# Kernel tuning notes

Measured on AMD Instinct MI355X. Metric: run time of the kernel, lower is better.

Reference implementation:

```python
import jax, jax.numpy as jnp
import numpy as np

ALPHA = 0.2  # LeakyReLU negative slope
NEG_INF = -9e15


def gat_layer(h, adj_mask, W, a, concat):
    # h: [N, F_in], W: [F_in, F_out], a: [2*F_out, 1]
    Wh = h @ W                                   # [N, F_out]
    f_out = W.shape[1]
    e1 = Wh @ a[:f_out]                          # [N, 1]
    e2 = Wh @ a[f_out:]                          # [N, 1]
    e = jax.nn.leaky_relu(e1 + e2.T, ALPHA)      # [N, N] pairwise scores
    att = jnp.where(adj_mask, e, NEG_INF)
    att = jax.nn.softmax(att, axis=1)            # masked row softmax
    h_prime = att @ Wh                           # [N, F_out] aggregate
    out = jax.nn.elu(h_prime) if concat else h_prime
    return out, att


def setup_inputs() -> dict:
    N, nfeat, nhid, nclass = 8192, 512, 256, 16
    key = jax.random.key(0)
    k = jax.random.split(key, 6)
    x = jax.random.normal(k[0], (N, nfeat), dtype=jnp.float32)
    adj = jax.random.randint(k[1], (N, N), 0, 2, dtype=jnp.int32)
    W1 = jax.random.normal(k[2], (nfeat, nhid), dtype=jnp.float32) * (1.0 / np.sqrt(nfeat))
    a1 = jax.random.normal(k[3], (2 * nhid, 1), dtype=jnp.float32) * 0.1
    W2 = jax.random.normal(k[4], (nhid, nclass), dtype=jnp.float32) * (1.0 / np.sqrt(nhid))
    a2 = jax.random.normal(k[5], (2 * nclass, 1), dtype=jnp.float32) * 0.1
    return {"x": x, "adj": adj, "W1": W1, "a1": a1, "W2": W2, "a2": a2}


def reference(x, adj, W1, a1, W2, a2):
    adj_mask = adj > 0
    # layer 1: attentions (concat=True -> ELU)
    h1, att1 = gat_layer(x, adj_mask, W1, a1, concat=True)
    # out layer (concat=False) + sigmoid
    h2, att2 = gat_layer(h1, adj_mask, W2, a2, concat=False)
    out = jax.nn.sigmoid(h2)
    # mirrors torch return: (x, gft_list, att_list, attention)
    return out, h1, att1, att2
```

## Files before the change

### kernel.cpp

```cpp
#include <hip/hip_runtime.h>
#include <hip/hip_bf16.h>

#define LRELU_ALPHA 0.2f

typedef __attribute__((ext_vector_type(8))) __bf16 bf16x8;
typedef __attribute__((ext_vector_type(4))) float f32x4;
typedef __attribute__((ext_vector_type(8))) unsigned short u16x8;
typedef __attribute__((ext_vector_type(4))) unsigned short u16x4;

__device__ __forceinline__ unsigned short f2bf(float f) {
  unsigned int u = __float_as_uint(f);
  u += 0x7fffu + ((u >> 16) & 1u);
  return (unsigned short)(u >> 16);
}

__global__ __launch_bounds__(256) void gemm_f32_k(
    const float* __restrict__ A, const float* __restrict__ B,
    float* __restrict__ C, int M, int K, int Ncols)
{
  __shared__ float As[128][17];
  __shared__ float Bs[16][65];
  int t = threadIdx.x;
  int row0 = blockIdx.x * 128;
  int col0 = blockIdx.y * 64;
  int ty = t >> 4, tx = t & 15;
  float acc[8][4];
#pragma unroll
  for (int i = 0; i < 8; ++i)
#pragma unroll
    for (int j = 0; j < 4; ++j) acc[i][j] = 0.f;

  for (int kt = 0; kt < K; kt += 16) {
    __syncthreads();
    {
      int r = t >> 1, h = t & 1;
      const float4* src = (const float4*)(A + (size_t)(row0 + r) * K + kt + h * 8);
      float4 v0 = src[0], v1 = src[1];
      float* dst = &As[r][h * 8];
      dst[0]=v0.x; dst[1]=v0.y; dst[2]=v0.z; dst[3]=v0.w;
      dst[4]=v1.x; dst[5]=v1.y; dst[6]=v1.z; dst[7]=v1.w;
    }
    {
      int kr = t >> 4, seg = t & 15;
      const float4* src = (const float4*)(B + (size_t)(kt + kr) * Ncols + col0 + seg * 4);
      float4 v = src[0];
      float* dst = &Bs[kr][seg * 4];
      dst[0]=v.x; dst[1]=v.y; dst[2]=v.z; dst[3]=v.w;
    }
    __syncthreads();
#pragma unroll
    for (int k = 0; k < 16; ++k) {
      float bb[4];
#pragma unroll
      for (int j = 0; j < 4; ++j) bb[j] = Bs[k][tx * 4 + j];
#pragma unroll
      for (int i = 0; i < 8; ++i) {
        float aa = As[ty * 8 + i][k];
#pragma unroll
        for (int j = 0; j < 4; ++j) acc[i][j] = fmaf(aa, bb[j], acc[i][j]);
      }
    }
  }
#pragma unroll
  for (int i = 0; i < 8; ++i) {
    float4 v = make_float4(acc[i][0], acc[i][1], acc[i][2], acc[i][3]);
    *(float4*)(C + (size_t)(row0 + ty * 8 + i) * Ncols + col0 + tx * 4) = v;
  }
}

__global__ __launch_bounds__(256) void calc_e_k(
    const float* __restrict__ Wh, const float* __restrict__ a,
    float* __restrict__ e1, float* __restrict__ e2, int F)
{
  int row = blockIdx.x * 4 + (threadIdx.x >> 6);
  int l = threadIdx.x & 63;
  const float* r = Wh + (size_t)row * F;
  float s1 = 0.f, s2 = 0.f;
  for (int f = l; f < F; f += 64) {
    float v = r[f];
    s1 += v * a[f];
    s2 += v * a[F + f];
  }
#pragma unroll
  for (int off = 32; off; off >>= 1) {
    s1 += __shfl_down(s1, off);
    s2 += __shfl_down(s2, off);
  }
  if (l == 0) { e1[row] = s1; e2[row] = s2; }
}

__global__ void transpose_bf16_k(const float* __restrict__ in, unsigned short* __restrict__ out,
                                 int R, int Cc)
{
  __shared__ float tile[32][33];
  int tx = threadIdx.x, ty = threadIdx.y;
  int c0 = blockIdx.x * 32, r0 = blockIdx.y * 32;
  int c = c0 + tx;
  if (c < Cc) {
    for (int i = ty; i < 32; i += 8)
      tile[i][tx] = in[(size_t)(r0 + i) * Cc + c];
  }
  __syncthreads();
  int r = r0 + tx;
  for (int i = ty; i < 32; i += 8) {
    int cc = c0 + i;
    if (cc < Cc)
      out[(size_t)cc * R + r] = f2bf(tile[tx][i]);
  }
}

__global__ __launch_bounds__(256) void att_softmax1_k(
    const int* __restrict__ adj, const float* __restrict__ e1,
    const float* __restrict__ e2, float* __restrict__ att,
    unsigned* __restrict__ bits)
{
  __shared__ float red[4];
  int i = blockIdx.x, t = threadIdx.x;
  const int4* arow = (const int4*)(adj + (size_t)i * 8192);
  unsigned* brow = bits + (size_t)i * 256;
  float e1i = e1[i];
  float4 vv[8];
  float s = 0.f;
#pragma unroll
  for (int it = 0; it < 8; ++it) {
    int j4 = t + it * 256;
    int4 a4 = arow[j4];
    float4 ev = *(const float4*)(e2 + j4 * 4);
    unsigned n = (unsigned)(a4.x > 0) | ((unsigned)(a4.y > 0) << 1)
               | ((unsigned)(a4.z > 0) << 2) | ((unsigned)(a4.w > 0) << 3);
    unsigned v = n << ((t & 7) * 4);
    v |= __shfl_xor(v, 1);
    v |= __shfl_xor(v, 2);
    v |= __shfl_xor(v, 4);
    if ((t & 7) == 0) brow[it * 32 + (t >> 3)] = v;
    float e, p0, p1, p2, p3;
    e = e1i + ev.x; e = e > 0.f ? e : LRELU_ALPHA * e; p0 = (a4.x > 0) ? __expf(e) : 0.f;
    e = e1i + ev.y; e = e > 0.f ? e : LRELU_ALPHA * e; p1 = (a4.y > 0) ? __expf(e) : 0.f;
    e = e1i + ev.z; e = e > 0.f ? e : LRELU_ALPHA * e; p2 = (a4.z > 0) ? __expf(e) : 0.f;
    e = e1i + ev.w; e = e > 0.f ? e : LRELU_ALPHA * e; p3 = (a4.w > 0) ? __expf(e) : 0.f;
    vv[it] = make_float4(p0, p1, p2, p3);
    s += (p0 + p1) + (p2 + p3);
  }
#pragma unroll
  for (int off = 32; off; off >>= 1) s += __shfl_xor(s, off);
  if ((t & 63) == 0) red[t >> 6] = s;
  __syncthreads();
  s = red[0] + red[1] + red[2] + red[3];
  float inv = 1.f / s;
  float4* orow = (float4*)(att + (size_t)i * 8192);
#pragma unroll
  for (int it = 0; it < 8; ++it) {
    float4 p = vv[it];
    p.x *= inv; p.y *= inv; p.z *= inv; p.w *= inv;
    orow[t + it * 256] = p;
  }
}

__global__ __launch_bounds__(256) void att_softmax2_k(
    const unsigned* __restrict__ bits, const float* __restrict__ e1,
    const float* __restrict__ e2, float* __restrict__ att)
{
  __shared__ unsigned bw[256];
  __shared__ float red[4];
  int i = blockIdx.x, t = threadIdx.x;
  bw[t] = bits[(size_t)i * 256 + t];
  float e1i = e1[i];
  __syncthreads();
  float4 vv[8];
  float s = 0.f;
#pragma unroll
  for (int it = 0; it < 8; ++it) {
    int j4 = t + it * 256;
    float4 ev = *(const float4*)(e2 + j4 * 4);
    unsigned wb = bw[j4 >> 3];
    int b0 = (j4 & 7) * 4;
    float e, p0, p1, p2, p3;
    e = e1i + ev.x; e = e > 0.f ? e : LRELU_ALPHA * e; p0 = ((wb >> (b0 + 0)) & 1) ? __expf(e) : 0.f;
    e = e1i + ev.y; e = e > 0.f ? e : LRELU_ALPHA * e; p1 = ((wb >> (b0 + 1)) & 1) ? __expf(e) : 0.f;
    e = e1i + ev.z; e = e > 0.f ? e : LRELU_ALPHA * e; p2 = ((wb >> (b0 + 2)) & 1) ? __expf(e) : 0.f;
    e = e1i + ev.w; e = e > 0.f ? e : LRELU_ALPHA * e; p3 = ((wb >> (b0 + 3)) & 1) ? __expf(e) : 0.f;
    vv[it] = make_float4(p0, p1, p2, p3);
    s += (p0 + p1) + (p2 + p3);
  }
#pragma unroll
  for (int off = 32; off; off >>= 1) s += __shfl_xor(s, off);
  if ((t & 63) == 0) red[t >> 6] = s;
  __syncthreads();
  s = red[0] + red[1] + red[2] + red[3];
  float inv = 1.f / s;
  float4* orow = (float4*)(att + (size_t)i * 8192);
#pragma unroll
  for (int it = 0; it < 8; ++it) {
    float4 p = vv[it];
    p.x *= inv; p.y *= inv; p.z *= inv; p.w *= inv;
    orow[t + it * 256] = p;
  }
}

template<int BN, int SPLITK, int EPI>
__global__ __launch_bounds__(256) void gemm_mfma_k(
    const float* __restrict__ A, const unsigned short* __restrict__ BT,
    float* __restrict__ Cout, int M, int K, int ldc)
{
  constexpr int BM = 64, BK = 64;
  constexpr int WN = (BN == 64) ? 2 : 1;
  constexpr int WM = 4 / WN;
  constexpr int WROWS = BM / WM;
  constexpr int WCOLS = BN / WN;
  constexpr int FM = WROWS / 16;
  constexpr int FN = WCOLS / 16;
  __shared__ __align__(16) char As[BM * BK * 2];
  __shared__ __align__(16) char Bs[BN * BK * 2];
  int t = threadIdx.x;
  int row0 = blockIdx.x * BM;
  int col0 = blockIdx.y * BN;
  int ktiles = K / BK;
  int kt0 = blockIdx.z * (ktiles / SPLITK);
  int kt1 = kt0 + ktiles / SPLITK;
  int w = t >> 6, l = t & 63;
  int wm = w / WN, wn = w % WN;

  f32x4 acc[FM][FN] = {};

  int ar = t >> 2, aseg = t & 3;
  int swzA = (ar & 7) << 4;

  for (int kt = kt0; kt < kt1; ++kt) {
    __syncthreads();
    {
      const float4* src = (const float4*)(A + (size_t)(row0 + ar) * K + kt * BK + aseg * 16);
      float4 v0 = src[0], v1 = src[1], v2 = src[2], v3 = src[3];
      u16x8 c0, c1;
      c0[0]=f2bf(v0.x); c0[1]=f2bf(v0.y); c0[2]=f2bf(v0.z); c0[3]=f2bf(v0.w);
      c0[4]=f2bf(v1.x); c0[5]=f2bf(v1.y); c0[6]=f2bf(v1.z); c0[7]=f2bf(v1.w);
      c1[0]=f2bf(v2.x); c1[1]=f2bf(v2.y); c1[2]=f2bf(v2.z); c1[3]=f2bf(v2.w);
      c1[4]=f2bf(v3.x); c1[5]=f2bf(v3.y); c1[6]=f2bf(v3.z); c1[7]=f2bf(v3.w);
      int base = ar * 128 + aseg * 32;
      *(u16x8*)(As + ((base) ^ swzA)) = c0;
      *(u16x8*)(As + ((base + 16) ^ swzA)) = c1;
    }
    if (BN == 64) {
      int br = t >> 2, seg = t & 3;
      const u16x8* src = (const u16x8*)(BT + (size_t)(col0 + br) * K + kt * BK + seg * 16);
      u16x8 b0 = src[0], b1 = src[1];
      int base = br * 128 + seg * 32;
      int swz = (br & 7) << 4;
      *(u16x8*)(Bs + ((base) ^ swz)) = b0;
      *(u16x8*)(Bs + ((base + 16) ^ swz)) = b1;
    } else {
      int br = t >> 4, seg = t & 15;
      const u16x4* src = (const u16x4*)(BT + (size_t)(col0 + br) * K + kt * BK + seg * 4);
      u16x4 b0 = src[0];
      int base = br * 128 + seg * 8;
      int swz = (br & 7) << 4;
      *(u16x4*)(Bs + (base ^ swz)) = b0;
    }
    __syncthreads();
#pragma unroll
    for (int kk = 0; kk < BK; kk += 32) {
      bf16x8 af[FM], bfr[FN];
      int kb = (kk + (l >> 4) * 8) * 2;
#pragma unroll
      for (int fm = 0; fm < FM; ++fm) {
        int r = wm * WROWS + fm * 16 + (l & 15);
        af[fm] = *(const bf16x8*)(As + ((r * 128 + kb) ^ ((r & 7) << 4)));
      }
#pragma unroll
      for (int fn = 0; fn < FN; ++fn) {
        int c = wn * WCOLS + fn * 16 + (l & 15);
        bfr[fn] = *(const bf16x8*)(Bs + ((c * 128 + kb) ^ ((c & 7) << 4)));
      }
#pragma unroll
      for (int fm = 0; fm < FM; ++fm)
#pragma unroll
        for (int fn = 0; fn < FN; ++fn)
          acc[fm][fn] = __builtin_amdgcn_mfma_f32_16x16x32_bf16(af[fm], bfr[fn], acc[fm][fn], 0, 0, 0);
    }
  }
#pragma unroll
  for (int fm = 0; fm < FM; ++fm) {
#pragma unroll
    for (int fn = 0; fn < FN; ++fn) {
#pragma unroll
      for (int r = 0; r < 4; ++r) {
        int grow = row0 + wm * WROWS + fm * 16 + (l >> 4) * 4 + r;
        int gcol = col0 + wn * WCOLS + fn * 16 + (l & 15);
        float v = acc[fm][fn][r];
        if (EPI == 1) v = v > 0.f ? v : expm1f(v);
        size_t idx = (SPLITK > 1)
          ? ((size_t)blockIdx.z * M + grow) * ldc + gcol
          : (size_t)grow * ldc + gcol;
        Cout[idx] = v;
      }
    }
  }
}

__global__ __launch_bounds__(256) void gemm_small_k(
    const float* __restrict__ A, const float* __restrict__ B,
    float* __restrict__ C, int K, int Ncols)
{
  int t = threadIdx.x;
  int r = blockIdx.x * 16 + (t >> 4);
  int c = t & 15;
  const float* arow = A + (size_t)r * K;
  float acc = 0.f;
#pragma unroll 8
  for (int k = 0; k < K; ++k)
    acc = fmaf(arow[k], B[k * Ncols + c], acc);
  C[(size_t)r * Ncols + c] = acc;
}

__global__ void reduce_elu_k(const float* __restrict__ part, float* __restrict__ out, int total)
{
  int i = blockIdx.x * 256 + threadIdx.x;
  if (i < total) {
    float s = (part[i] + part[total + i]) + (part[2 * (size_t)total + i] + part[3 * (size_t)total + i]);
    out[i] = s > 0.f ? s : expm1f(s);
  }
}

__global__ void reduce_sig16_k(const float* __restrict__ part, float* __restrict__ out, int total)
{
  int i = blockIdx.x * 256 + threadIdx.x;
  if (i < total) {
    float s = 0.f;
#pragma unroll
    for (int z = 0; z < 16; ++z)
      s += part[(size_t)z * total + i];
    out[i] = 1.f / (1.f + __expf(-s));
  }
}

extern "C" void kernel_launch(void* const* d_in, const int* in_sizes, int n_in,
                              void* d_out, int out_size, void* d_ws, size_t ws_size,
                              hipStream_t stream)
{
  const float* x   = (const float*)d_in[0];
  const int*   adj = (const int*)d_in[1];
  const float* W1  = (const float*)d_in[2];
  const float* a1  = (const float*)d_in[3];
  const float* W2  = (const float*)d_in[4];
  const float* a2  = (const float*)d_in[5];

  float* out  = (float*)d_out;
  float* h1   = out + 131072;
  float* att1 = h1 + 2097152;
  float* att2 = att1 + 67108864;

  float* ws = (float*)d_ws;
  float* wh1 = ws;
  unsigned short* bt1 = (unsigned short*)(wh1 + 2097152);
  float* e1a = wh1 + 2097152 + 1048576;
  float* e2a = e1a + 8192;
  float* wh2 = e2a + 8192;
  unsigned short* bt2 = (unsigned short*)(wh2 + 131072);
  float* e1b = wh2 + 131072 + 65536;
  float* e2b = e1b + 8192;
  float* part2 = e2b + 8192;
  unsigned* bits = (unsigned*)(part2 + 2097152);
  float* part1 = (float*)(bits + 2097152);

  gemm_f32_k<<<dim3(64, 4), 256, 0, stream>>>(x, W1, wh1, 8192, 512, 256);
  calc_e_k<<<2048, 256, 0, stream>>>(wh1, a1, e1a, e2a, 256);
  transpose_bf16_k<<<dim3(8, 256), dim3(32, 8), 0, stream>>>(wh1, bt1, 8192, 256);
  att_softmax1_k<<<8192, 256, 0, stream>>>(adj, e1a, e2a, att1, bits);
  gemm_mfma_k<64, 4, 0><<<dim3(128, 4, 4), 256, 0, stream>>>(att1, bt1, part1, 8192, 8192, 256);
  reduce_elu_k<<<8192, 256, 0, stream>>>(part1, h1, 2097152);

  gemm_small_k<<<512, 256, 0, stream>>>(h1, W2, wh2, 256, 16);
  calc_e_k<<<2048, 256, 0, stream>>>(wh2, a2, e1b, e2b, 16);
  transpose_bf16_k<<<dim3(1, 256), dim3(32, 8), 0, stream>>>(wh2, bt2, 8192, 16);
  att_softmax2_k<<<8192, 256, 0, stream>>>(bits, e1b, e2b, att2);
  gemm_mfma_k<16, 16, 0><<<dim3(128, 1, 16), 256, 0, stream>>>(att2, bt2, part2, 8192, 8192, 16);
  reduce_sig16_k<<<512, 256, 0, stream>>>(part2, out, 131072);
}
```

Before: 460.8 us.

## Fuse layer-1 attention softmax into aggregation GEMM using a row-sum pre-pass

The layer-1 softmax kernel now only computes the packed adjacency bits and the inverse row sums. A new fused kernel rebuilds the normalized attention values from the bits, e1 and e2 tile by tile. It writes them to the att1 output and also converts them to bf16 in shared memory to feed MFMA directly, so the aggregation GEMM no longer reads the full fp32 att1 matrix back from memory. Split-K goes from 4 to 8, and the reduction kernel is adjusted to match. The exp work is done twice, the partial-sum buffer doubles, and the fused loop has no load/compute overlap.

```diff
diff --git a/kernel.cpp b/kernel.cpp
--- a/kernel.cpp
+++ b/kernel.cpp
@@ -109,17 +109,16 @@
   }
 }
 
-__global__ __launch_bounds__(256) void att_softmax1_k(
+__global__ __launch_bounds__(256) void rowsum_pack_k(
     const int* __restrict__ adj, const float* __restrict__ e1,
-    const float* __restrict__ e2, float* __restrict__ att,
-    unsigned* __restrict__ bits)
+    const float* __restrict__ e2, unsigned* __restrict__ bits,
+    float* __restrict__ sinv)
 {
   __shared__ float red[4];
   int i = blockIdx.x, t = threadIdx.x;
   const int4* arow = (const int4*)(adj + (size_t)i * 8192);
   unsigned* brow = bits + (size_t)i * 256;
   float e1i = e1[i];
-  float4 vv[8];
   float s = 0.f;
 #pragma unroll
   for (int it = 0; it < 8; ++it) {
@@ -133,26 +132,111 @@
     v |= __shfl_xor(v, 2);
     v |= __shfl_xor(v, 4);
     if ((t & 7) == 0) brow[it * 32 + (t >> 3)] = v;
-    float e, p0, p1, p2, p3;
-    e = e1i + ev.x; e = e > 0.f ? e : LRELU_ALPHA * e; p0 = (a4.x > 0) ? __expf(e) : 0.f;
-    e = e1i + ev.y; e = e > 0.f ? e : LRELU_ALPHA * e; p1 = (a4.y > 0) ? __expf(e) : 0.f;
-    e = e1i + ev.z; e = e > 0.f ? e : LRELU_ALPHA * e; p2 = (a4.z > 0) ? __expf(e) : 0.f;
-    e = e1i + ev.w; e = e > 0.f ? e : LRELU_ALPHA * e; p3 = (a4.w > 0) ? __expf(e) : 0.f;
-    vv[it] = make_float4(p0, p1, p2, p3);
-    s += (p0 + p1) + (p2 + p3);
+    float e;
+    e = e1i + ev.x; e = e > 0.f ? e : LRELU_ALPHA * e; s += (a4.x > 0) ? __expf(e) : 0.f;
+    e = e1i + ev.y; e = e > 0.f ? e : LRELU_ALPHA * e; s += (a4.y > 0) ? __expf(e) : 0.f;
+    e = e1i + ev.z; e = e > 0.f ? e : LRELU_ALPHA * e; s += (a4.z > 0) ? __expf(e) : 0.f;
+    e = e1i + ev.w; e = e > 0.f ? e : LRELU_ALPHA * e; s += (a4.w > 0) ? __expf(e) : 0.f;
   }
 #pragma unroll
   for (int off = 32; off; off >>= 1) s += __shfl_xor(s, off);
   if ((t & 63) == 0) red[t >> 6] = s;
   __syncthreads();
-  s = red[0] + red[1] + red[2] + red[3];
-  float inv = 1.f / s;
-  float4* orow = (float4*)(att + (size_t)i * 8192);
-#pragma unroll
-  for (int it = 0; it < 8; ++it) {
-    float4 p = vv[it];
-    p.x *= inv; p.y *= inv; p.z *= inv; p.w *= inv;
-    orow[t + it * 256] = p;
+  if (t == 0) sinv[i] = 1.f / (red[0] + red[1] + red[2] + red[3]);
+}
+
+__global__ __launch_bounds__(256) void fused_att_agg1_k(
+    const unsigned* __restrict__ bits, const float* __restrict__ e1,
+    const float* __restrict__ e2, const float* __restrict__ sinv,
+    const unsigned short* __restrict__ BT,
+    float* __restrict__ att, float* __restrict__ part)
+{
+  __shared__ __align__(16) char As[64 * 128];
+  __shared__ __align__(16) char Bs[256 * 128];
+  int t = threadIdx.x;
+  int l = t & 63, w = t >> 6;
+  int row0 = blockIdx.x * 64;
+  int z = blockIdx.y;
+  int wm = w >> 1, wn = w & 1;
+
+  f32x4 acc[2][8] = {};
+
+  int pr = t >> 2, seg = t & 3;
+  float e1v = e1[row0 + pr];
+  float siv = sinv[row0 + pr];
+  const unsigned* brow = bits + (size_t)(row0 + pr) * 256 + z * 32;
+  const float* e2p = e2 + z * 1024;
+  float* arow_att = att + (size_t)(row0 + pr) * 8192 + z * 1024;
+  int abase = pr * 128 + seg * 32;
+  int aswz = (pr & 7) << 4;
+
+  const unsigned short* bgp = BT + (size_t)t * 8192 + z * 1024;
+  int bbase = t * 128;
+  int bswz = (t & 7) << 4;
+
+  for (int kt = 0; kt < 16; ++kt) {
+    __syncthreads();
+    {
+      const u16x8* src = (const u16x8*)(bgp + kt * 64);
+#pragma unroll
+      for (int s = 0; s < 8; ++s)
+        *(u16x8*)(Bs + ((bbase + s * 16) ^ bswz)) = src[s];
+    }
+    {
+      int j0 = kt * 64 + seg * 16;
+      unsigned mb = brow[kt * 2 + (seg >> 1)] >> ((seg & 1) * 16);
+      float p[16];
+#pragma unroll
+      for (int q = 0; q < 4; ++q) {
+        float4 ev = *(const float4*)(e2p + j0 + q * 4);
+        float e;
+        e = e1v + ev.x; e = e > 0.f ? e : LRELU_ALPHA * e;
+        p[q*4+0] = ((mb >> (q*4+0)) & 1) ? __expf(e) * siv : 0.f;
+        e = e1v + ev.y; e = e > 0.f ? e : LRELU_ALPHA * e;
+        p[q*4+1] = ((mb >> (q*4+1)) & 1) ? __expf(e) * siv : 0.f;
+        e = e1v + ev.z; e = e > 0.f ? e : LRELU_ALPHA * e;
+        p[q*4+2] = ((mb >> (q*4+2)) & 1) ? __expf(e) * siv : 0.f;
+        e = e1v + ev.w; e = e > 0.f ? e : LRELU_ALPHA * e;
+        p[q*4+3] = ((mb >> (q*4+3)) & 1) ? __expf(e) * siv : 0.f;
+        *(float4*)(arow_att + j0 + q * 4) = make_float4(p[q*4+0], p[q*4+1], p[q*4+2], p[q*4+3]);
+      }
+      u16x8 c0, c1;
+#pragma unroll
+      for (int q = 0; q < 8; ++q) { c0[q] = f2bf(p[q]); c1[q] = f2bf(p[8 + q]); }
+      *(u16x8*)(As + ((abase) ^ aswz)) = c0;
+      *(u16x8*)(As + ((abase + 16) ^ aswz)) = c1;
+    }
+    __syncthreads();
+#pragma unroll
+    for (int kk = 0; kk < 64; kk += 32) {
+      int kb = (kk + (l >> 4) * 8) * 2;
+      bf16x8 af[2];
+#pragma unroll
+      for (int fm = 0; fm < 2; ++fm) {
+        int r = wm * 32 + fm * 16 + (l & 15);
+        af[fm] = *(const bf16x8*)(As + ((r * 128 + kb) ^ ((r & 7) << 4)));
+      }
+#pragma unroll
+      for (int fn = 0; fn < 8; ++fn) {
+        int c = wn * 128 + fn * 16 + (l & 15);
+        bf16x8 bf = *(const bf16x8*)(Bs + ((c * 128 + kb) ^ ((c & 7) << 4)));
+#pragma unroll
+        for (int fm = 0; fm < 2; ++fm)
+          acc[fm][fn] = __builtin_amdgcn_mfma_f32_16x16x32_bf16(af[fm], bf, acc[fm][fn], 0, 0, 0);
+      }
+    }
+  }
+#pragma unroll
+  for (int fm = 0; fm < 2; ++fm) {
+#pragma unroll
+    for (int fn = 0; fn < 8; ++fn) {
+#pragma unroll
+      for (int r = 0; r < 4; ++r) {
+        int grow = row0 + wm * 32 + fm * 16 + (l >> 4) * 4 + r;
+        int gcol = wn * 128 + fn * 16 + (l & 15);
+        part[((size_t)z * 8192 + grow) * 256 + gcol] = acc[fm][fn][r];
+      }
+    }
   }
 }
 
@@ -311,11 +395,14 @@
   C[(size_t)r * Ncols + c] = acc;
 }
 
-__global__ void reduce_elu_k(const float* __restrict__ part, float* __restrict__ out, int total)
+__global__ void reduce_elu8_k(const float* __restrict__ part, float* __restrict__ out, int total)
 {
   int i = blockIdx.x * 256 + threadIdx.x;
   if (i < total) {
-    float s = (part[i] + part[total + i]) + (part[2 * (size_t)total + i] + part[3 * (size_t)total + i]);
+    float s = 0.f;
+#pragma unroll
+    for (int z = 0; z < 8; ++z)
+      s += part[(size_t)z * total + i];
     out[i] = s > 0.f ? s : expm1f(s);
   }
 }
@@ -353,7 +440,8 @@
   unsigned short* bt1 = (unsigned short*)(wh1 + 2097152);
   float* e1a = wh1 + 2097152 + 1048576;
   float* e2a = e1a + 8192;
-  float* wh2 = e2a + 8192;
+  float* sinv1 = e2a + 8192;
+  float* wh2 = sinv1 + 8192;
   unsigned short* bt2 = (unsigned short*)(wh2 + 131072);
   float* e1b = wh2 + 131072 + 65536;
   float* e2b = e1b + 8192;
@@ -364,9 +452,9 @@
   gemm_f32_k<<<dim3(64, 4), 256, 0, stream>>>(x, W1, wh1, 8192, 512, 256);
   calc_e_k<<<2048, 256, 0, stream>>>(wh1, a1, e1a, e2a, 256);
   transpose_bf16_k<<<dim3(8, 256), dim3(32, 8), 0, stream>>>(wh1, bt1, 8192, 256);
-  att_softmax1_k<<<8192, 256, 0, stream>>>(adj, e1a, e2a, att1, bits);
-  gemm_mfma_k<64, 4, 0><<<dim3(128, 4, 4), 256, 0, stream>>>(att1, bt1, part1, 8192, 8192, 256);
-  reduce_elu_k<<<8192, 256, 0, stream>>>(part1, h1, 2097152);
+  rowsum_pack_k<<<8192, 256, 0, stream>>>(adj, e1a, e2a, bits, sinv1);
+  fused_att_agg1_k<<<dim3(128, 8), 256, 0, stream>>>(bits, e1a, e2a, sinv1, bt1, att1, part1);
+  reduce_elu8_k<<<8192, 256, 0, stream>>>(part1, h1, 2097152);
 
   gemm_small_k<<<512, 256, 0, stream>>>(h1, W2, wh2, 256, 16);
   calc_e_k<<<2048, 256, 0, stream>>>(wh2, a2, e1b, e2b, 16);
```

Result: slower. 566.2 us (+22.9%).
